# Performance work log

Hardware: AMD Instinct MI355X
Metric: run time of the kernel (lower is better)

Reference implementation:

```python
import jax, jax.numpy as jnp
import numpy as np
from jax import lax

T = 8
TAU = 2.0
ALPHA = 4.0   # spikingjelly surrogate.Sigmoid default alpha
EPS = 1e-5


def _kaiming(key, shape, fan_in):
    return jax.random.normal(key, shape, jnp.float32) * np.sqrt(2.0 / fan_in)


def setup_inputs() -> dict:
    key = jax.random.key(0)
    ks = jax.random.split(key, 16)
    d = {}
    d['x'] = jax.random.normal(ks[0], (128, 3, 32, 32), jnp.float32)
    convs = [('1', 32, 3), ('2', 32, 32), ('3', 64, 32), ('4', 64, 64), ('5', 128, 64), ('6', 128, 128)]
    for i, (s, co, ci) in enumerate(convs):
        d['w' + s] = _kaiming(ks[1 + i], (co, ci, 3, 3), ci * 9)
        d['b' + s] = jnp.zeros((co,), jnp.float32)
        d['g' + s] = jnp.ones((co,), jnp.float32)
        d['be' + s] = jnp.zeros((co,), jnp.float32)
    d['fc1_w'] = _kaiming(ks[7], (128, 2048), 2048)
    d['fc1_b'] = jnp.zeros((128,), jnp.float32)
    d['fc2_w'] = _kaiming(ks[8], (10, 128), 128)
    d['fc2_b'] = jnp.zeros((10,), jnp.float32)
    return d


def _conv2d(x, w, b):  # x [M,C,H,W], w [O,I,3,3], pad=1 stride=1
    y = lax.conv_general_dilated(x, w, (1, 1), ((1, 1), (1, 1)),
                                 dimension_numbers=('NCHW', 'OIHW', 'NCHW'))
    return y + b[None, :, None, None]


def _bn(x, g, be):  # training-mode BN over merged (T*N,H,W) batch
    m = x.mean(axis=(0, 2, 3))
    v = x.var(axis=(0, 2, 3))
    inv = g / jnp.sqrt(v + EPS)
    return x * inv[None, :, None, None] + (be - m * inv)[None, :, None, None]


def _lif(x_seq, th):
    # spikingjelly LIFNode defaults: decay_input=True, v_reset=0 (hard reset),
    # surrogate sigmoid gradient. x_seq: [T, ...]
    def step(v, x):
        v = v + (x - v) / TAU
        sig = jax.nn.sigmoid(ALPHA * (v - th))
        hard = (v >= th).astype(x.dtype)
        spike = lax.stop_gradient(hard - sig) + sig  # fwd: heaviside, bwd: sigmoid'
        return v * (1.0 - spike), spike
    return lax.scan(step, jnp.zeros_like(x_seq[0]), x_seq)[1]


def _maxpool(x):  # [M,C,H,W] -> 2x2 stride 2
    return lax.reduce_window(x, -jnp.inf, lax.max, (1, 1, 2, 2), (1, 1, 2, 2), 'VALID')


def _cbl(xs, w, b, g, be, th):  # conv-bn over merged TN, LIF scan over T
    t, n = xs.shape[0], xs.shape[1]
    m = xs.reshape((t * n,) + xs.shape[2:])
    y = _bn(_conv2d(m, w, b), g, be)
    return _lif(y.reshape((t, n) + y.shape[1:]), th)


def _pool_seq(xs):
    t, n = xs.shape[0], xs.shape[1]
    y = _maxpool(xs.reshape((t * n,) + xs.shape[2:]))
    return y.reshape((t, n) + y.shape[1:])


def _forward(x, w1, b1, g1, be1, w2, b2, g2, be2, w3, b3, g3, be3,
             w4, b4, g4, be4, w5, b5, g5, be5, w6, b6, g6, be6,
             fc1_w, fc1_b, fc2_w, fc2_b):
    th = 1.0
    xs = jnp.broadcast_to(x[None], (T,) + x.shape)  # [T,N,3,32,32]
    xs = _cbl(xs, w1, b1, g1, be1, th)
    xs = _cbl(xs, w2, b2, g2, be2, th)
    xs = _pool_seq(xs)                                # [T,N,32,16,16]
    xs = _cbl(xs, w3, b3, g3, be3, th)
    xs = _cbl(xs, w4, b4, g4, be4, th)
    xs = _pool_seq(xs)                                # [T,N,64,8,8]
    xs = _cbl(xs, w5, b5, g5, be5, th)
    xs = _cbl(xs, w6, b6, g6, be6, th)
    xs = _pool_seq(xs)                                # [T,N,128,4,4]
    t, n = xs.shape[0], xs.shape[1]
    f = xs.reshape(t, n, -1)                          # [T,N,2048]
    h = jnp.einsum('tnf,of->tno', f, fc1_w) + fc1_b
    h = _lif(h, 1.0)
    o = jnp.einsum('tnf,of->tno', h, fc2_w) + fc2_b
    o = _lif(o, 1.0)
    return o.mean(axis=0)                             # [N,10]


def reference(x, w1, b1, g1, be1, w2, b2, g2, be2, w3, b3, g3, be3,
              w4, b4, g4, be4, w5, b5, g5, be5, w6, b6, g6, be6,
              fc1_w, fc1_b, fc2_w, fc2_b):
    return _forward(x, w1, b1, g1, be1, w2, b2, g2, be2, w3, b3, g3, be3,
                    w4, b4, g4, be4, w5, b5, g5, be5, w6, b6, g6, be6,
                    fc1_w, fc1_b, fc2_w, fc2_b)
```

## Files before the change

kernel.cpp:

```cpp
#include <hip/hip_runtime.h>
#include <stdint.h>


#define T_STEPS 8
#define NBATCH 128

typedef __attribute__((ext_vector_type(8))) short short8;
typedef __attribute__((ext_vector_type(4))) float f32x4;

__device__ __forceinline__ uint16_t f2bf(float f) {
    uint32_t x = __float_as_uint(f);
    uint32_t r = x + 0x7FFFu + ((x >> 16) & 1u);
    return (uint16_t)(r >> 16);
}
__device__ __forceinline__ float bf2f(uint16_t h) {
    return __uint_as_float(((uint32_t)h) << 16);
}

__global__ void zero_kernel(float* p, int n) {
    int i = blockIdx.x * blockDim.x + threadIdx.x;
    if (i < n) p[i] = 0.0f;
}

template <int C, int HP, int WPP>
__global__ void border_kernel(uint16_t* __restrict__ s, int nimg) {
    constexpr int NB = 2 * WPP + 2 * (HP - 2);
    constexpr int C2 = C / 2;
    constexpr int PX = C + 8;
    const int i = blockIdx.x * blockDim.x + threadIdx.x;
    if (i >= nimg * NB * C2) return;
    const int c2 = i % C2;
    const int b = (i / C2) % NB;
    const int img = i / (C2 * NB);
    int py, px;
    if (b < WPP) { py = 0; px = b; }
    else if (b < 2 * WPP) { py = HP - 1; px = b - WPP; }
    else { const int r = b - 2 * WPP; py = 1 + (r >> 1); px = (r & 1) ? (WPP - 1) : 0; }
    *(uint32_t*)&s[(size_t)img * (HP * WPP * PX) + (py * WPP + px) * PX + 2 * c2] = 0u;
}

template <int CIN, int COUT>
__global__ void prep_kernel(const float* __restrict__ w, uint16_t* __restrict__ wp) {
    constexpr int KC = CIN / 32;
    const int i = blockIdx.x * blockDim.x + threadIdx.x;
    if (i >= COUT * CIN * 9) return;
    const int sh = i % 9;
    const int ci = (i / 9) % CIN;
    const int co = i / (9 * CIN);
    const float v = w[i];
    const uint16_t h1 = f2bf(v);
    const float r1 = v - bf2f(h1);
    const uint16_t h2 = f2bf(r1);
    const float r2 = r1 - bf2f(h2);
    const uint16_t h3 = f2bf(r2);
    uint16_t* base = wp + (size_t)((co >> 4) * KC + (ci >> 5)) * 14976
                        + sh * 1664 + (co & 15) * 104 + (ci & 31);
    base[0] = h1;
    base[32] = h2;
    base[64] = h3;
}

__global__ void prep_fc1_kernel(const float* __restrict__ w, uint16_t* __restrict__ wp) {
    const int i = blockIdx.x * blockDim.x + threadIdx.x;
    if (i >= 128 * 2048) return;
    const int kp = i & 2047;
    const int o = i >> 11;
    const int px = kp >> 7, c = kp & 127;
    const float v = w[o * 2048 + c * 16 + px];
    const uint16_t h1 = f2bf(v);
    const float r1 = v - bf2f(h1);
    const uint16_t h2 = f2bf(r1);
    const float r2 = r1 - bf2f(h2);
    const uint16_t h3 = f2bf(r2);
    uint16_t* base = wp + (size_t)((o >> 4) * 64 + (kp >> 5)) * 1664
                        + (o & 15) * 104 + (kp & 31);
    base[0] = h1;
    base[32] = h2;
    base[64] = h3;
}

__global__ void conv3x3_kernel(const float* __restrict__ in,
                               const float* __restrict__ wgt,
                               const float* __restrict__ bias,
                               float* __restrict__ y,
                               float* __restrict__ ssum,
                               float* __restrict__ ssq,
                               int Cin, int H, int W) {
    const int m  = blockIdx.x;
    const int co = blockIdx.y;
    const int Cout = gridDim.y;
    const int HW = H * W;

    const float* wco = wgt + (size_t)co * Cin * 9;
    const float bv = bias[co];

    float lsum = 0.0f, lsq = 0.0f;

    for (int p = threadIdx.x; p < HW; p += blockDim.x) {
        const int hy = p / W;
        const int wx = p - hy * W;
        float acc = bv;
        for (int ci = 0; ci < Cin; ++ci) {
            const float* inc = in + ((size_t)m * Cin + ci) * HW;
            const float* wc = wco + ci * 9;
#pragma unroll
            for (int ky = 0; ky < 3; ++ky) {
                const int iy = hy + ky - 1;
                if (iy < 0 || iy >= H) continue;
#pragma unroll
                for (int kx = 0; kx < 3; ++kx) {
                    const int ix = wx + kx - 1;
                    if (ix < 0 || ix >= W) continue;
                    acc += inc[iy * W + ix] * wc[ky * 3 + kx];
                }
            }
        }
        y[((size_t)m * HW + p) * Cout + co] = acc;
        lsum += acc;
        lsq += acc * acc;
    }

    __shared__ float r1[256];
    __shared__ float r2[256];
    const int tid = threadIdx.x;
    r1[tid] = lsum;
    r2[tid] = lsq;
    __syncthreads();
    for (int s = blockDim.x >> 1; s > 0; s >>= 1) {
        if (tid < s) {
            r1[tid] += r1[tid + s];
            r2[tid] += r2[tid + s];
        }
        __syncthreads();
    }
    if (tid == 0) {
        atomicAdd(&ssum[co], r1[0]);
        atomicAdd(&ssq[co], r2[0]);
    }
}

template <int CIN, int COUT, int H, int W, int ROWS, int IMPB, int NCO, int KSPLIT>
__global__ __launch_bounds__(256) void conv_mfma_kernel(
    const uint16_t* __restrict__ in, const uint16_t* __restrict__ wp,
    const float* __restrict__ bias, float* __restrict__ y,
    float* __restrict__ ssum, float* __restrict__ ssq)
{
    constexpr int KC = CIN / 32;
    constexpr int WPP = W + 2;
    constexpr int HW = H * W;
    constexpr int PXU16 = CIN + 8;
    constexpr int ISTR = (H + 2) * WPP * PXU16;
    constexpr int RB = H / ROWS;
    constexpr int NSTRIP = IMPB * ROWS * W / 16;
    constexpr int MSPLIT = 4 / KSPLIT;
    constexpr int SPW = NSTRIP / MSPLIT;
    constexpr int TILE_U16 = IMPB * (ROWS + 2) * WPP * PXU16;
    constexpr int NIT = KC * 9;
    constexpr int ITW = NIT / KSPLIT;
    constexpr int CS = NCO * 16 + 1;
    static_assert(IMPB == 1 || ROWS == H, "impb needs full-image tiles");
    static_assert(NSTRIP % MSPLIT == 0 && NSTRIP % 4 == 0, "strips");
    static_assert(NIT % KSPLIT == 0, "ksplit");
    static_assert(TILE_U16 % 8 == 0, "tile f4");
    static_assert(KSPLIT == 1 || TILE_U16 * 2 >= NSTRIP * 16 * CS * 4, "C fits");

    __shared__ __align__(16) uint16_t sp[TILE_U16];
    __shared__ float bn[NCO * 32];

    const int tid = threadIdx.x;
    const int lane = tid & 63;
    const int wav = tid >> 6;
    const int kg = wav / MSPLIT;
    const int mg = wav - kg * MSPLIT;
    const int col = lane & 15;
    const int quad = lane >> 4;

    const int m0 = (blockIdx.x / RB) * IMPB;
    const int ybase = (blockIdx.x % RB) * ROWS;

    if (tid < NCO * 32) bn[tid] = 0.0f;

    {
        const float4* src = (const float4*)(in + (size_t)m0 * ISTR
                                               + (size_t)ybase * WPP * PXU16);
        float4* dst = (float4*)sp;
        for (int i = tid; i < TILE_U16 / 8; i += 256) dst[i] = src[i];
    }
    __syncthreads();

    int abase[SPW];
#pragma unroll
    for (int s = 0; s < SPW; ++s) {
        const int p = (mg * SPW + s) * 16 + col;
        const int img = p / (ROWS * W);
        const int rem = p % (ROWS * W);
        abase[s] = ((img * (ROWS + 2) + rem / W) * WPP + rem % W) * PXU16 + quad * 8;
    }

    f32x4 acc[SPW][NCO];
#pragma unroll
    for (int s = 0; s < SPW; ++s)
#pragma unroll
        for (int j = 0; j < NCO; ++j) acc[s][j] = (f32x4)0.0f;

    const uint16_t* wbase = wp + ((size_t)blockIdx.y * NCO * KC) * 14976
                               + col * 104 + quad * 8;

    auto loadB = [&](short8 (&buf)[NCO][3], int it) {
        const int kc = it / 9, sh = it - kc * 9;
#pragma unroll
        for (int j = 0; j < NCO; ++j) {
            const uint16_t* p = wbase + (size_t)(j * KC + kc) * 14976 + sh * 1664;
            buf[j][0] = *(const short8*)p;
            buf[j][1] = *(const short8*)(p + 32);
            buf[j][2] = *(const short8*)(p + 64);
        }
    };
    auto mfmaStep = [&](short8 (&buf)[NCO][3], int it) {
        const int kc = it / 9, sh = it - kc * 9;
        const int dy = sh / 3, dx = sh - dy * 3;
        const int shoff = (dy * WPP + dx) * PXU16 + kc * 32;
#pragma unroll
        for (int s = 0; s < SPW; ++s) {
            const short8 a = *(const short8*)&sp[abase[s] + shoff];
#pragma unroll
            for (int j = 0; j < NCO; ++j) {
                f32x4 t = acc[s][j];
                t = __builtin_amdgcn_mfma_f32_16x16x32_bf16(a, buf[j][0], t, 0, 0, 0);
                t = __builtin_amdgcn_mfma_f32_16x16x32_bf16(a, buf[j][1], t, 0, 0, 0);
                t = __builtin_amdgcn_mfma_f32_16x16x32_bf16(a, buf[j][2], t, 0, 0, 0);
                acc[s][j] = t;
            }
        }
    };

    short8 bufA[NCO][3], bufB[NCO][3];
    const int it0 = kg * ITW, it1 = it0 + ITW;
    loadB(bufA, it0);
    int it = it0;
#pragma unroll 1
    for (; it + 2 <= it1; it += 2) {
        loadB(bufB, it + 1);
        mfmaStep(bufA, it);
        if (it + 2 < it1) loadB(bufA, it + 2);
        mfmaStep(bufB, it + 1);
    }
    if (it < it1) mfmaStep(bufA, it);

    if constexpr (KSPLIT == 1) {
#pragma unroll
        for (int j = 0; j < NCO; ++j) {
            const int co0 = (blockIdx.y * NCO + j) * 16;
            const float bv = bias[co0 + col];
#pragma unroll
            for (int s = 0; s < SPW; ++s) {
                const int pb_ = (mg * SPW + s) * 16 + quad * 4;
                float sum = 0.0f, sq = 0.0f;
#pragma unroll
                for (int r = 0; r < 4; ++r) {
                    const float v = acc[s][j][r] + bv;
                    const int p = pb_ + r;
                    const int img = p / (ROWS * W);
                    const int pxim = p % (ROWS * W) + ybase * W;
                    y[((size_t)(m0 + img) * HW + pxim) * COUT + co0 + col] = v;
                    sum += v;
                    sq += v * v;
                }
                sum += __shfl_xor(sum, 16, 64);
                sum += __shfl_xor(sum, 32, 64);
                sq += __shfl_xor(sq, 16, 64);
                sq += __shfl_xor(sq, 32, 64);
                if (quad == 0) {
                    atomicAdd(&bn[j * 32 + col], sum);
                    atomicAdd(&bn[j * 32 + 16 + col], sq);
                }
            }
        }
    } else {
        float* Csh = (float*)sp;
        __syncthreads();
        if (kg == 0) {
#pragma unroll
            for (int s = 0; s < SPW; ++s)
#pragma unroll
                for (int j = 0; j < NCO; ++j)
#pragma unroll
                    for (int r = 0; r < 4; ++r)
                        Csh[((mg * SPW + s) * 16 + quad * 4 + r) * CS + j * 16 + col]
                            = acc[s][j][r];
        }
        __syncthreads();
#pragma unroll
        for (int k = 1; k < KSPLIT; ++k) {
            if (kg == k) {
#pragma unroll
                for (int s = 0; s < SPW; ++s)
#pragma unroll
                    for (int j = 0; j < NCO; ++j)
#pragma unroll
                        for (int r = 0; r < 4; ++r)
                            Csh[((mg * SPW + s) * 16 + quad * 4 + r) * CS + j * 16 + col]
                                += acc[s][j][r];
            }
            __syncthreads();
        }
        constexpr int ES = NSTRIP / 4;
#pragma unroll
        for (int s2 = 0; s2 < ES; ++s2) {
            const int gs = wav * ES + s2;
#pragma unroll
            for (int j = 0; j < NCO; ++j) {
                const int co0 = (blockIdx.y * NCO + j) * 16;
                const float bv = bias[co0 + col];
                float sum = 0.0f, sq = 0.0f;
#pragma unroll
                for (int r = 0; r < 4; ++r) {
                    const float v = Csh[(gs * 16 + quad * 4 + r) * CS + j * 16 + col] + bv;
                    const int p = gs * 16 + quad * 4 + r;
                    const int img = p / (ROWS * W);
                    const int pxim = p % (ROWS * W) + ybase * W;
                    y[((size_t)(m0 + img) * HW + pxim) * COUT + co0 + col] = v;
                    sum += v;
                    sq += v * v;
                }
                sum += __shfl_xor(sum, 16, 64);
                sum += __shfl_xor(sum, 32, 64);
                sq += __shfl_xor(sq, 16, 64);
                sq += __shfl_xor(sq, 32, 64);
                if (quad == 0) {
                    atomicAdd(&bn[j * 32 + col], sum);
                    atomicAdd(&bn[j * 32 + 16 + col], sq);
                }
            }
        }
    }
    __syncthreads();
    if (tid < NCO * 32) {
        const int j = tid >> 5, r = tid & 31;
        const int co0 = (blockIdx.y * NCO + j) * 16;
        if (r < 16) atomicAdd(&ssum[co0 + r], bn[j * 32 + r]);
        else atomicAdd(&ssq[co0 + r - 16], bn[j * 32 + r]);
    }
}

__global__ void bnlif1_pad_kernel(const float* __restrict__ y,
                                  const float* __restrict__ ssum,
                                  const float* __restrict__ ssq,
                                  const float* __restrict__ g,
                                  const float* __restrict__ be,
                                  uint16_t* __restrict__ s, float invM) {
    constexpr int OSTR = 34 * 34 * 40;
    const int i = blockIdx.x * blockDim.x + threadIdx.x;
    if (i >= NBATCH * 1024 * 16) return;
    const int c2 = i % 16;
    const int px = (i / 16) % 1024;
    const int n = i / (16 * 1024);
    const int c0 = 2 * c2;
    const float m0 = ssum[c0] * invM, m1 = ssum[c0 + 1] * invM;
    const float inv0 = g[c0] / sqrtf(ssq[c0] * invM - m0 * m0 + 1e-5f);
    const float inv1 = g[c0 + 1] / sqrtf(ssq[c0 + 1] * invM - m1 * m1 + 1e-5f);
    const float2 zz = *(const float2*)&y[((size_t)n * 1024 + px) * 32 + c0];
    const float z0 = zz.x * inv0 + (be[c0] - m0 * inv0);
    const float z1 = zz.y * inv1 + (be[c0 + 1] - m1 * inv1);
    const int pyy = px >> 5, pxx = px & 31;
    const size_t obase = (size_t)n * OSTR + ((pyy + 1) * 34 + pxx + 1) * 40 + c0;
    const size_t otstride = (size_t)NBATCH * OSTR;
    float v0 = 0.0f, v1 = 0.0f;
#pragma unroll
    for (int t = 0; t < T_STEPS; ++t) {
        v0 += (z0 - v0) * 0.5f;
        v1 += (z1 - v1) * 0.5f;
        const uint32_t b0 = v0 >= 1.0f, b1 = v1 >= 1.0f;
        *(uint32_t*)&s[t * otstride + obase] = (b0 | (b1 << 16)) * 0x3F80u;
        if (b0) v0 = 0.0f;
        if (b1) v1 = 0.0f;
    }
}

template <int C, int H, int W>
__global__ void bnlif_pad_kernel(const float* __restrict__ y,
                                 const float* __restrict__ ssum,
                                 const float* __restrict__ ssq,
                                 const float* __restrict__ g,
                                 const float* __restrict__ be,
                                 uint16_t* __restrict__ s, float invM) {
    constexpr int C2 = C / 2;
    constexpr int HW = H * W;
    constexpr int OSTR = (H + 2) * (W + 2) * (C + 8);
    const int i = blockIdx.x * blockDim.x + threadIdx.x;
    if (i >= NBATCH * HW * C2) return;
    const int c2 = i % C2;
    const int px = (i / C2) % HW;
    const int n = i / (C2 * HW);
    const int c0 = 2 * c2;
    const float m0 = ssum[c0] * invM, m1 = ssum[c0 + 1] * invM;
    const float inv0 = g[c0] / sqrtf(ssq[c0] * invM - m0 * m0 + 1e-5f);
    const float inv1 = g[c0 + 1] / sqrtf(ssq[c0 + 1] * invM - m1 * m1 + 1e-5f);
    const float sh0 = be[c0] - m0 * inv0;
    const float sh1 = be[c0 + 1] - m1 * inv1;
    const size_t ybase = ((size_t)n * HW + px) * C + c0;
    const size_t tstride = (size_t)NBATCH * HW * C;
    const int pyy = px / W, pxx = px % W;
    const size_t obase = (size_t)n * OSTR + ((pyy + 1) * (W + 2) + pxx + 1) * (C + 8) + c0;
    const size_t otstride = (size_t)NBATCH * OSTR;
    float v0 = 0.0f, v1 = 0.0f;
#pragma unroll
    for (int t = 0; t < T_STEPS; ++t) {
        const float2 zz = *(const float2*)&y[t * tstride + ybase];
        const float z0 = zz.x * inv0 + sh0;
        const float z1 = zz.y * inv1 + sh1;
        v0 += (z0 - v0) * 0.5f;
        v1 += (z1 - v1) * 0.5f;
        const uint32_t b0 = v0 >= 1.0f, b1 = v1 >= 1.0f;
        *(uint32_t*)&s[t * otstride + obase] = (b0 | (b1 << 16)) * 0x3F80u;
        if (b0) v0 = 0.0f;
        if (b1) v1 = 0.0f;
    }
}

template <int C, int H, int W>
__global__ void bnlifpool_pad_kernel(const float* __restrict__ y,
                                     const float* __restrict__ ssum,
                                     const float* __restrict__ ssq,
                                     const float* __restrict__ g,
                                     const float* __restrict__ be,
                                     uint16_t* __restrict__ s, float invM) {
    constexpr int C2 = C / 2;
    constexpr int PH = H / 2, PW = W / 2;
    constexpr int OSTR = (PH + 2) * (PW + 2) * (C + 8);
    const int i = blockIdx.x * blockDim.x + threadIdx.x;
    if (i >= NBATCH * PH * PW * C2) return;
    const int c2 = i % C2;
    const int pw = (i / C2) % PW;
    const int ph = (i / (C2 * PW)) % PH;
    const int n = i / (C2 * PW * PH);
    const int c0 = 2 * c2;
    const float m0 = ssum[c0] * invM, m1 = ssum[c0 + 1] * invM;
    const float inv0 = g[c0] / sqrtf(ssq[c0] * invM - m0 * m0 + 1e-5f);
    const float inv1 = g[c0 + 1] / sqrtf(ssq[c0 + 1] * invM - m1 * m1 + 1e-5f);
    const float sh0 = be[c0] - m0 * inv0;
    const float sh1 = be[c0 + 1] - m1 * inv1;
    const size_t base = (((size_t)n * H + 2 * ph) * W + 2 * pw) * C + c0;
    const size_t tstride = (size_t)NBATCH * H * W * C;
    const size_t obase = (size_t)n * OSTR + ((ph + 1) * (PW + 2) + pw + 1) * (C + 8) + c0;
    const size_t otstride = (size_t)NBATCH * OSTR;
    float a0 = 0.f, a1 = 0.f, a2 = 0.f, a3 = 0.f;
    float b0_ = 0.f, b1_ = 0.f, b2_ = 0.f, b3_ = 0.f;
#pragma unroll
    for (int t = 0; t < T_STEPS; ++t) {
        const float* yt = y + t * tstride + base;
        const float2 p00 = *(const float2*)&yt[0];
        const float2 p01 = *(const float2*)&yt[C];
        const float2 p10 = *(const float2*)&yt[(size_t)W * C];
        const float2 p11 = *(const float2*)&yt[(size_t)W * C + C];
        a0 += (p00.x * inv0 + sh0 - a0) * 0.5f;
        a1 += (p01.x * inv0 + sh0 - a1) * 0.5f;
        a2 += (p10.x * inv0 + sh0 - a2) * 0.5f;
        a3 += (p11.x * inv0 + sh0 - a3) * 0.5f;
        b0_ += (p00.y * inv1 + sh1 - b0_) * 0.5f;
        b1_ += (p01.y * inv1 + sh1 - b1_) * 0.5f;
        b2_ += (p10.y * inv1 + sh1 - b2_) * 0.5f;
        b3_ += (p11.y * inv1 + sh1 - b3_) * 0.5f;
        const uint32_t sa0 = a0 >= 1.0f, sa1 = a1 >= 1.0f, sa2 = a2 >= 1.0f, sa3 = a3 >= 1.0f;
        const uint32_t sb0 = b0_ >= 1.0f, sb1 = b1_ >= 1.0f, sb2 = b2_ >= 1.0f, sb3 = b3_ >= 1.0f;
        if (sa0) a0 = 0.0f;
        if (sa1) a1 = 0.0f;
        if (sa2) a2 = 0.0f;
        if (sa3) a3 = 0.0f;
        if (sb0) b0_ = 0.0f;
        if (sb1) b1_ = 0.0f;
        if (sb2) b2_ = 0.0f;
        if (sb3) b3_ = 0.0f;
        const uint32_t pa = sa0 | sa1 | sa2 | sa3;
        const uint32_t pbt = sb0 | sb1 | sb2 | sb3;
        *(uint32_t*)&s[t * otstride + obase] = (pa | (pbt << 16)) * 0x3F80u;
    }
}

__global__ __launch_bounds__(256) void fc1_mfma_kernel(
    const uint16_t* __restrict__ f, const uint16_t* __restrict__ wfc,
    const float* __restrict__ b, float* __restrict__ h)
{
    __shared__ __align__(16) uint16_t A[16 * 2056];
    const int tid = threadIdx.x;
    const int lane = tid & 63, wav = tid >> 6;
    const int col = lane & 15, quad = lane >> 4;
    const int r0 = blockIdx.x * 16;

    {
        const int row = tid >> 4, px = tid & 15;
        const int py = px >> 2, pxx = px & 3;
        const float4* src = (const float4*)(f + (size_t)(r0 + row) * 4896
                                            + ((py + 1) * 6 + pxx + 1) * 136);
        float4* dst = (float4*)&A[row * 2056 + px * 128];
#pragma unroll
        for (int i = 0; i < 16; ++i) dst[i] = src[i];
    }
    __syncthreads();

    const int coblk = blockIdx.y * 4 + wav;
    const uint16_t* wbase = wfc + (size_t)coblk * 64 * 1664 + col * 104 + quad * 8;
    f32x4 acc = (f32x4)0.0f;

    auto loadB = [&](short8 (&buf)[3], int kc) {
        const uint16_t* p = wbase + kc * 1664;
        buf[0] = *(const short8*)p;
        buf[1] = *(const short8*)(p + 32);
        buf[2] = *(const short8*)(p + 64);
    };
    auto step = [&](short8 (&buf)[3], int kc) {
        const short8 a = *(const short8*)&A[col * 2056 + kc * 32 + quad * 8];
        acc = __builtin_amdgcn_mfma_f32_16x16x32_bf16(a, buf[0], acc, 0, 0, 0);
        acc = __builtin_amdgcn_mfma_f32_16x16x32_bf16(a, buf[1], acc, 0, 0, 0);
        acc = __builtin_amdgcn_mfma_f32_16x16x32_bf16(a, buf[2], acc, 0, 0, 0);
    };

    short8 bA[3], bB[3];
    loadB(bA, 0);
#pragma unroll 1
    for (int kc = 0; kc + 2 <= 64; kc += 2) {
        loadB(bB, kc + 1);
        step(bA, kc);
        if (kc + 2 < 64) loadB(bA, kc + 2);
        step(bB, kc + 1);
    }

    const int o = coblk * 16 + col;
    const float bv = b[o];
#pragma unroll
    for (int r = 0; r < 4; ++r)
        h[(size_t)(r0 + quad * 4 + r) * 128 + o] = acc[r] + bv;
}

__global__ void lif_fc_kernel(const float* __restrict__ h,
                              uint8_t* __restrict__ s, int NF) {
    const int i = blockIdx.x * blockDim.x + threadIdx.x;
    if (i >= NF) return;
    float v = 0.0f;
#pragma unroll
    for (int t = 0; t < T_STEPS; ++t) {
        const float z = h[(size_t)t * NF + i];
        v += (z - v) * 0.5f;
        const float sp = (v >= 1.0f) ? 1.0f : 0.0f;
        s[(size_t)t * NF + i] = (uint8_t)sp;
        v *= (1.0f - sp);
    }
}

__global__ void fc2_kernel(const uint8_t* __restrict__ sh,
                           const float* __restrict__ w,
                           const float* __restrict__ b,
                           float* __restrict__ out) {
    const int i = blockIdx.x * blockDim.x + threadIdx.x;
    if (i >= NBATCH * 10) return;
    const int k = i % 10;
    const int n = i / 10;
    float v = 0.0f, acc = 0.0f;
    for (int t = 0; t < T_STEPS; ++t) {
        const uint8_t* row = sh + ((size_t)t * NBATCH + n) * 128;
        float z = b[k];
        for (int o = 0; o < 128; ++o)
            z += (float)row[o] * w[k * 128 + o];
        v += (z - v) * 0.5f;
        const float sp = (v >= 1.0f) ? 1.0f : 0.0f;
        acc += sp;
        v *= (1.0f - sp);
    }
    out[i] = acc * (1.0f / T_STEPS);
}

extern "C" void kernel_launch(void* const* d_in, const int* in_sizes, int n_in,
                              void* d_out, int out_size, void* d_ws, size_t ws_size,
                              hipStream_t stream) {
    const float* x   = (const float*)d_in[0];
    const float* W1  = (const float*)d_in[1];
    const float* Bi1 = (const float*)d_in[2];
    const float* G1  = (const float*)d_in[3];
    const float* BE1 = (const float*)d_in[4];
    const float* W2  = (const float*)d_in[5];
    const float* Bi2 = (const float*)d_in[6];
    const float* G2  = (const float*)d_in[7];
    const float* BE2 = (const float*)d_in[8];
    const float* W3  = (const float*)d_in[9];
    const float* Bi3 = (const float*)d_in[10];
    const float* G3  = (const float*)d_in[11];
    const float* BE3 = (const float*)d_in[12];
    const float* W4  = (const float*)d_in[13];
    const float* Bi4 = (const float*)d_in[14];
    const float* G4  = (const float*)d_in[15];
    const float* BE4 = (const float*)d_in[16];
    const float* W5  = (const float*)d_in[17];
    const float* Bi5 = (const float*)d_in[18];
    const float* G5  = (const float*)d_in[19];
    const float* BE5 = (const float*)d_in[20];
    const float* W6  = (const float*)d_in[21];
    const float* Bi6 = (const float*)d_in[22];
    const float* G6  = (const float*)d_in[23];
    const float* BE6 = (const float*)d_in[24];
    const float* FC1W = (const float*)d_in[25];
    const float* FC1B = (const float*)d_in[26];
    const float* FC2W = (const float*)d_in[27];
    const float* FC2B = (const float*)d_in[28];

    uint8_t* ws = (uint8_t*)d_ws;
    float*    Y   = (float*)ws;
    const size_t S1OFF = 134217728;
    uint16_t* S1 = (uint16_t*)(ws + S1OFF);
    uint16_t* S2 = (uint16_t*)(ws + S1OFF);
    uint16_t* S3 = (uint16_t*)(ws + S1OFF + 26542080);
    uint16_t* S4 = (uint16_t*)(ws + S1OFF);
    uint16_t* S5 = (uint16_t*)(ws + S1OFF + 14745600);
    uint16_t* S6 = (uint16_t*)(ws + S1OFF + 42598400);
    float*    stats = (float*)(ws + S1OFF + 94699520);
    float*    h     = (float*)(ws + S1OFF + 94699520 + 8192);
    uint8_t*  shb   = ws + S1OFF + 94699520 + 8192 + 524288;
    uint16_t* Wp    = (uint16_t*)(shb + 131072);
    uint16_t* Wp2p = Wp;
    uint16_t* Wp3p = Wp + 29952;
    uint16_t* Wp4p = Wp + 89856;
    uint16_t* Wp5p = Wp + 209664;
    uint16_t* Wp6p = Wp + 449280;
    uint16_t* Wfc1 = Wp + 928512;

    zero_kernel<<<(1536 + 255) / 256, 256, 0, stream>>>(stats, 1536);

    prep_kernel<32, 32><<<(9216 + 255) / 256, 256, 0, stream>>>(W2, Wp2p);
    prep_kernel<32, 64><<<(18432 + 255) / 256, 256, 0, stream>>>(W3, Wp3p);
    prep_kernel<64, 64><<<(36864 + 255) / 256, 256, 0, stream>>>(W4, Wp4p);
    prep_kernel<64, 128><<<(73728 + 255) / 256, 256, 0, stream>>>(W5, Wp5p);
    prep_kernel<128, 128><<<(147456 + 255) / 256, 256, 0, stream>>>(W6, Wp6p);
    prep_fc1_kernel<<<(262144) / 256, 256, 0, stream>>>(FC1W, Wfc1);

    const int TN = T_STEPS * NBATCH;

    border_kernel<32, 34, 34><<<(1024 * 132 * 16 + 255) / 256, 256, 0, stream>>>(S1, 1024);
    border_kernel<32, 18, 18><<<(1024 * 68 * 16 + 255) / 256, 256, 0, stream>>>(S2, 1024);
    border_kernel<64, 18, 18><<<(1024 * 68 * 32 + 255) / 256, 256, 0, stream>>>(S3, 1024);
    border_kernel<64, 10, 10><<<(1024 * 36 * 32 + 255) / 256, 256, 0, stream>>>(S4, 1024);
    border_kernel<128, 10, 10><<<(1024 * 36 * 64 + 255) / 256, 256, 0, stream>>>(S5, 1024);
    border_kernel<128, 6, 6><<<(1024 * 20 * 64 + 255) / 256, 256, 0, stream>>>(S6, 1024);

    {
        dim3 g(NBATCH, 32);
        conv3x3_kernel<<<g, 256, 0, stream>>>(x, W1, Bi1, Y,
                                              stats + 0, stats + 128, 3, 32, 32);
        bnlif1_pad_kernel<<<(NBATCH * 1024 * 16 + 255) / 256, 256, 0, stream>>>(
            Y, stats + 0, stats + 128, G1, BE1, S1, 1.0f / 131072.0f);
    }
    {
        conv_mfma_kernel<32, 32, 32, 32, 16, 1, 2, 1><<<dim3(TN * 2, 1), 256, 0, stream>>>(
            S1, Wp2p, Bi2, Y, stats + 256, stats + 384);
        bnlifpool_pad_kernel<32, 32, 32><<<(NBATCH * 16 * 16 * 16 + 255) / 256, 256, 0, stream>>>(
            Y, stats + 256, stats + 384, G2, BE2, S2, 1.0f / (1024.0f * 1024.0f));
    }
    {
        conv_mfma_kernel<32, 64, 16, 16, 16, 2, 1, 1><<<dim3(TN / 2, 4), 256, 0, stream>>>(
            S2, Wp3p, Bi3, Y, stats + 512, stats + 640);
        bnlif_pad_kernel<64, 16, 16><<<(NBATCH * 256 * 32 + 255) / 256, 256, 0, stream>>>(
            Y, stats + 512, stats + 640, G3, BE3, S3, 1.0f / (1024.0f * 256.0f));
    }
    {
        conv_mfma_kernel<64, 64, 16, 16, 16, 1, 1, 2><<<dim3(TN, 4), 256, 0, stream>>>(
            S3, Wp4p, Bi4, Y, stats + 768, stats + 896);
        bnlifpool_pad_kernel<64, 16, 16><<<(NBATCH * 8 * 8 * 32 + 255) / 256, 256, 0, stream>>>(
            Y, stats + 768, stats + 896, G4, BE4, S4, 1.0f / (1024.0f * 256.0f));
    }
    {
        conv_mfma_kernel<64, 128, 8, 8, 8, 2, 2, 2><<<dim3(TN / 2, 4), 256, 0, stream>>>(
            S4, Wp5p, Bi5, Y, stats + 1024, stats + 1152);
        bnlif_pad_kernel<128, 8, 8><<<(NBATCH * 64 * 64 + 255) / 256, 256, 0, stream>>>(
            Y, stats + 1024, stats + 1152, G5, BE5, S5, 1.0f / (1024.0f * 64.0f));
    }
    {
        conv_mfma_kernel<128, 128, 8, 8, 8, 2, 2, 4><<<dim3(TN / 2, 4), 256, 0, stream>>>(
            S5, Wp6p, Bi6, Y, stats + 1280, stats + 1408);
        bnlifpool_pad_kernel<128, 8, 8><<<(NBATCH * 4 * 4 * 64 + 255) / 256, 256, 0, stream>>>(
            Y, stats + 1280, stats + 1408, G6, BE6, S6, 1.0f / (1024.0f * 64.0f));
    }
    fc1_mfma_kernel<<<dim3(64, 2), 256, 0, stream>>>(S6, Wfc1, FC1B, h);
    lif_fc_kernel<<<(NBATCH * 128 + 255) / 256, 256, 0, stream>>>(h, shb, NBATCH * 128);
    fc2_kernel<<<(NBATCH * 10 + 255) / 256, 256, 0, stream>>>(shb, FC2W, FC2B, (float*)d_out);
}
```

Before: 719.3 us.

## Store spike maps as packed bytes and expand to bf16 in shared memory

Spike activations between layers are now stored as one byte per channel with no channel padding, instead of bf16 with 8 extra channels per pixel. Conv and fc1 kernels read 16-byte chunks and expand each byte to bf16 0/1 while filling shared memory, and the BN/LIF kernels now handle four channels per thread. The weight-prep and border-zeroing launches are each merged into one kernel, and NCO is retuned for conv3/conv4. This cuts activation traffic to roughly half, at the cost of extra unpacking ALU work and shared-memory stores during tile loads.

New measurement: 691.7 us. 3.8% less time.

```diff
diff --git a/kernel.cpp b/kernel.cpp
--- a/kernel.cpp
+++ b/kernel.cpp
@@ -22,37 +22,22 @@
     if (i < n) p[i] = 0.0f;
 }
 
-template <int C, int HP, int WPP>
-__global__ void border_kernel(uint16_t* __restrict__ s, int nimg) {
-    constexpr int NB = 2 * WPP + 2 * (HP - 2);
-    constexpr int C2 = C / 2;
-    constexpr int PX = C + 8;
-    const int i = blockIdx.x * blockDim.x + threadIdx.x;
-    if (i >= nimg * NB * C2) return;
-    const int c2 = i % C2;
-    const int b = (i / C2) % NB;
-    const int img = i / (C2 * NB);
-    int py, px;
-    if (b < WPP) { py = 0; px = b; }
-    else if (b < 2 * WPP) { py = HP - 1; px = b - WPP; }
-    else { const int r = b - 2 * WPP; py = 1 + (r >> 1); px = (r & 1) ? (WPP - 1) : 0; }
-    *(uint32_t*)&s[(size_t)img * (HP * WPP * PX) + (py * WPP + px) * PX + 2 * c2] = 0u;
-}
-
-template <int CIN, int COUT>
-__global__ void prep_kernel(const float* __restrict__ w, uint16_t* __restrict__ wp) {
-    constexpr int KC = CIN / 32;
-    const int i = blockIdx.x * blockDim.x + threadIdx.x;
-    if (i >= COUT * CIN * 9) return;
+__device__ __forceinline__ void tsplit(float v, uint16_t& h1, uint16_t& h2, uint16_t& h3) {
+    h1 = f2bf(v);
+    const float r1 = v - bf2f(h1);
+    h2 = f2bf(r1);
+    const float r2 = r1 - bf2f(h2);
+    h3 = f2bf(r2);
+}
+
+__device__ __forceinline__ void prep_conv_one(const float* __restrict__ w,
+                                              uint16_t* __restrict__ wp, int i, int CIN) {
+    const int KC = CIN >> 5;
     const int sh = i % 9;
     const int ci = (i / 9) % CIN;
     const int co = i / (9 * CIN);
-    const float v = w[i];
-    const uint16_t h1 = f2bf(v);
-    const float r1 = v - bf2f(h1);
-    const uint16_t h2 = f2bf(r1);
-    const float r2 = r1 - bf2f(h2);
-    const uint16_t h3 = f2bf(r2);
+    uint16_t h1, h2, h3;
+    tsplit(w[i], h1, h2, h3);
     uint16_t* base = wp + (size_t)((co >> 4) * KC + (ci >> 5)) * 14976
                         + sh * 1664 + (co & 15) * 104 + (ci & 31);
     base[0] = h1;
@@ -60,23 +45,62 @@
     base[64] = h3;
 }
 
-__global__ void prep_fc1_kernel(const float* __restrict__ w, uint16_t* __restrict__ wp) {
-    const int i = blockIdx.x * blockDim.x + threadIdx.x;
-    if (i >= 128 * 2048) return;
+__device__ __forceinline__ void prep_fc1_one(const float* __restrict__ w,
+                                             uint16_t* __restrict__ wp, int i) {
     const int kp = i & 2047;
     const int o = i >> 11;
     const int px = kp >> 7, c = kp & 127;
-    const float v = w[o * 2048 + c * 16 + px];
-    const uint16_t h1 = f2bf(v);
-    const float r1 = v - bf2f(h1);
-    const uint16_t h2 = f2bf(r1);
-    const float r2 = r1 - bf2f(h2);
-    const uint16_t h3 = f2bf(r2);
+    uint16_t h1, h2, h3;
+    tsplit(w[o * 2048 + c * 16 + px], h1, h2, h3);
     uint16_t* base = wp + (size_t)((o >> 4) * 64 + (kp >> 5)) * 1664
                         + (o & 15) * 104 + (kp & 31);
     base[0] = h1;
     base[32] = h2;
     base[64] = h3;
+}
+
+__global__ void prep_all_kernel(const float* __restrict__ W2, const float* __restrict__ W3,
+                                const float* __restrict__ W4, const float* __restrict__ W5,
+                                const float* __restrict__ W6, const float* __restrict__ F1,
+                                uint16_t* __restrict__ P2, uint16_t* __restrict__ P3,
+                                uint16_t* __restrict__ P4, uint16_t* __restrict__ P5,
+                                uint16_t* __restrict__ P6, uint16_t* __restrict__ PF) {
+    int i = blockIdx.x * blockDim.x + threadIdx.x;
+    if (i < 9216) { prep_conv_one(W2, P2, i, 32); return; }
+    i -= 9216;
+    if (i < 18432) { prep_conv_one(W3, P3, i, 32); return; }
+    i -= 18432;
+    if (i < 36864) { prep_conv_one(W4, P4, i, 64); return; }
+    i -= 36864;
+    if (i < 73728) { prep_conv_one(W5, P5, i, 64); return; }
+    i -= 73728;
+    if (i < 147456) { prep_conv_one(W6, P6, i, 128); return; }
+    i -= 147456;
+    if (i < 262144) prep_fc1_one(F1, PF, i);
+}
+
+__global__ void border_all_kernel(uint8_t* S1, uint8_t* S2, uint8_t* S3,
+                                  uint8_t* S4, uint8_t* S5, uint8_t* S6) {
+    int i = blockIdx.x * blockDim.x + threadIdx.x;
+    uint8_t* s;
+    int C, HP, WPP;
+    if (i < 1081344) { s = S1; C = 32; HP = 34; WPP = 34; }
+    else if ((i -= 1081344) < 557056) { s = S2; C = 32; HP = 18; WPP = 18; }
+    else if ((i -= 557056) < 1114112) { s = S3; C = 64; HP = 18; WPP = 18; }
+    else if ((i -= 1114112) < 589824) { s = S4; C = 64; HP = 10; WPP = 10; }
+    else if ((i -= 589824) < 1179648) { s = S5; C = 128; HP = 10; WPP = 10; }
+    else if ((i -= 1179648) < 655360) { s = S6; C = 128; HP = 6; WPP = 6; }
+    else return;
+    const int C4 = C >> 2;
+    const int NB = 2 * WPP + 2 * (HP - 2);
+    const int c4 = i % C4;
+    const int b = (i / C4) % NB;
+    const int img = i / (C4 * NB);
+    int py, px;
+    if (b < WPP) { py = 0; px = b; }
+    else if (b < 2 * WPP) { py = HP - 1; px = b - WPP; }
+    else { const int r = b - 2 * WPP; py = 1 + (r >> 1); px = (r & 1) ? (WPP - 1) : 0; }
+    *(uint32_t*)&s[(size_t)img * (HP * WPP * C) + (py * WPP + px) * C + 4 * c4] = 0u;
 }
 
 __global__ void conv3x3_kernel(const float* __restrict__ in,
@@ -141,7 +165,7 @@
 
 template <int CIN, int COUT, int H, int W, int ROWS, int IMPB, int NCO, int KSPLIT>
 __global__ __launch_bounds__(256) void conv_mfma_kernel(
-    const uint16_t* __restrict__ in, const uint16_t* __restrict__ wp,
+    const uint8_t* __restrict__ in, const uint16_t* __restrict__ wp,
     const float* __restrict__ bias, float* __restrict__ y,
     float* __restrict__ ssum, float* __restrict__ ssq)
 {
@@ -149,19 +173,20 @@
     constexpr int WPP = W + 2;
     constexpr int HW = H * W;
     constexpr int PXU16 = CIN + 8;
-    constexpr int ISTR = (H + 2) * WPP * PXU16;
+    constexpr int ISTR_B = (H + 2) * WPP * CIN;
     constexpr int RB = H / ROWS;
     constexpr int NSTRIP = IMPB * ROWS * W / 16;
     constexpr int MSPLIT = 4 / KSPLIT;
     constexpr int SPW = NSTRIP / MSPLIT;
     constexpr int TILE_U16 = IMPB * (ROWS + 2) * WPP * PXU16;
+    constexpr int TILE_B = IMPB * (ROWS + 2) * WPP * CIN;
     constexpr int NIT = KC * 9;
     constexpr int ITW = NIT / KSPLIT;
     constexpr int CS = NCO * 16 + 1;
     static_assert(IMPB == 1 || ROWS == H, "impb needs full-image tiles");
     static_assert(NSTRIP % MSPLIT == 0 && NSTRIP % 4 == 0, "strips");
     static_assert(NIT % KSPLIT == 0, "ksplit");
-    static_assert(TILE_U16 % 8 == 0, "tile f4");
+    static_assert(TILE_B % 16 == 0, "tile u8 16B");
     static_assert(KSPLIT == 1 || TILE_U16 * 2 >= NSTRIP * 16 * CS * 4, "C fits");
 
     __shared__ __align__(16) uint16_t sp[TILE_U16];
@@ -181,10 +206,22 @@
     if (tid < NCO * 32) bn[tid] = 0.0f;
 
     {
-        const float4* src = (const float4*)(in + (size_t)m0 * ISTR
-                                               + (size_t)ybase * WPP * PXU16);
-        float4* dst = (float4*)sp;
-        for (int i = tid; i < TILE_U16 / 8; i += 256) dst[i] = src[i];
+        const uint8_t* src = in + (size_t)m0 * ISTR_B + (size_t)ybase * WPP * CIN;
+        for (int i = tid; i < TILE_B / 16; i += 256) {
+            const uint4 v = ((const uint4*)src)[i];
+            const int b = i * 16;
+            const int px = b / CIN;
+            const int ci = b - px * CIN;
+            uint32_t* d = (uint32_t*)&sp[px * PXU16 + ci];
+            d[0] = ((v.x & 1u) | (((v.x >> 8) & 1u) << 16)) * 0x3F80u;
+            d[1] = (((v.x >> 16) & 1u) | (((v.x >> 24) & 1u) << 16)) * 0x3F80u;
+            d[2] = ((v.y & 1u) | (((v.y >> 8) & 1u) << 16)) * 0x3F80u;
+            d[3] = (((v.y >> 16) & 1u) | (((v.y >> 24) & 1u) << 16)) * 0x3F80u;
+            d[4] = ((v.z & 1u) | (((v.z >> 8) & 1u) << 16)) * 0x3F80u;
+            d[5] = (((v.z >> 16) & 1u) | (((v.z >> 24) & 1u) << 16)) * 0x3F80u;
+            d[6] = ((v.w & 1u) | (((v.w >> 8) & 1u) << 16)) * 0x3F80u;
+            d[7] = (((v.w >> 16) & 1u) | (((v.w >> 24) & 1u) << 16)) * 0x3F80u;
+        }
     }
     __syncthreads();
 
@@ -348,32 +385,36 @@
                                   const float* __restrict__ ssq,
                                   const float* __restrict__ g,
                                   const float* __restrict__ be,
-                                  uint16_t* __restrict__ s, float invM) {
-    constexpr int OSTR = 34 * 34 * 40;
+                                  uint8_t* __restrict__ s, float invM) {
+    constexpr int OSTR = 34 * 34 * 32;
     const int i = blockIdx.x * blockDim.x + threadIdx.x;
-    if (i >= NBATCH * 1024 * 16) return;
-    const int c2 = i % 16;
-    const int px = (i / 16) % 1024;
-    const int n = i / (16 * 1024);
-    const int c0 = 2 * c2;
-    const float m0 = ssum[c0] * invM, m1 = ssum[c0 + 1] * invM;
-    const float inv0 = g[c0] / sqrtf(ssq[c0] * invM - m0 * m0 + 1e-5f);
-    const float inv1 = g[c0 + 1] / sqrtf(ssq[c0 + 1] * invM - m1 * m1 + 1e-5f);
-    const float2 zz = *(const float2*)&y[((size_t)n * 1024 + px) * 32 + c0];
-    const float z0 = zz.x * inv0 + (be[c0] - m0 * inv0);
-    const float z1 = zz.y * inv1 + (be[c0 + 1] - m1 * inv1);
+    if (i >= NBATCH * 1024 * 8) return;
+    const int c4 = i & 7;
+    const int px = (i >> 3) & 1023;
+    const int n = i >> 13;
+    const int c0 = 4 * c4;
+    float z[4], v[4];
+    const float4 q = *(const float4*)&y[((size_t)n * 1024 + px) * 32 + c0];
+    const float* qf = (const float*)&q;
+#pragma unroll
+    for (int c = 0; c < 4; ++c) {
+        const float m = ssum[c0 + c] * invM;
+        const float inv = g[c0 + c] / sqrtf(ssq[c0 + c] * invM - m * m + 1e-5f);
+        z[c] = qf[c] * inv + (be[c0 + c] - m * inv);
+        v[c] = 0.0f;
+    }
     const int pyy = px >> 5, pxx = px & 31;
-    const size_t obase = (size_t)n * OSTR + ((pyy + 1) * 34 + pxx + 1) * 40 + c0;
-    const size_t otstride = (size_t)NBATCH * OSTR;
-    float v0 = 0.0f, v1 = 0.0f;
+    const size_t obase = (size_t)n * OSTR + ((pyy + 1) * 34 + pxx + 1) * 32 + c0;
+    const size_t ot = (size_t)NBATCH * OSTR;
 #pragma unroll
     for (int t = 0; t < T_STEPS; ++t) {
-        v0 += (z0 - v0) * 0.5f;
-        v1 += (z1 - v1) * 0.5f;
-        const uint32_t b0 = v0 >= 1.0f, b1 = v1 >= 1.0f;
-        *(uint32_t*)&s[t * otstride + obase] = (b0 | (b1 << 16)) * 0x3F80u;
-        if (b0) v0 = 0.0f;
-        if (b1) v1 = 0.0f;
+        uint32_t pk = 0;
+#pragma unroll
+        for (int c = 0; c < 4; ++c) {
+            v[c] += (z[c] - v[c]) * 0.5f;
+            if (v[c] >= 1.0f) { v[c] = 0.0f; pk |= 1u << (8 * c); }
+        }
+        *(uint32_t*)&s[t * ot + obase] = pk;
     }
 }
 
@@ -383,38 +424,41 @@
                                  const float* __restrict__ ssq,
                                  const float* __restrict__ g,
                                  const float* __restrict__ be,
-                                 uint16_t* __restrict__ s, float invM) {
-    constexpr int C2 = C / 2;
+                                 uint8_t* __restrict__ s, float invM) {
+    constexpr int C4 = C / 4;
     constexpr int HW = H * W;
-    constexpr int OSTR = (H + 2) * (W + 2) * (C + 8);
+    constexpr int OSTR = (H + 2) * (W + 2) * C;
     const int i = blockIdx.x * blockDim.x + threadIdx.x;
-    if (i >= NBATCH * HW * C2) return;
-    const int c2 = i % C2;
-    const int px = (i / C2) % HW;
-    const int n = i / (C2 * HW);
-    const int c0 = 2 * c2;
-    const float m0 = ssum[c0] * invM, m1 = ssum[c0 + 1] * invM;
-    const float inv0 = g[c0] / sqrtf(ssq[c0] * invM - m0 * m0 + 1e-5f);
-    const float inv1 = g[c0 + 1] / sqrtf(ssq[c0 + 1] * invM - m1 * m1 + 1e-5f);
-    const float sh0 = be[c0] - m0 * inv0;
-    const float sh1 = be[c0 + 1] - m1 * inv1;
+    if (i >= NBATCH * HW * C4) return;
+    const int c4 = i % C4;
+    const int px = (i / C4) % HW;
+    const int n = i / (C4 * HW);
+    const int c0 = 4 * c4;
+    float inv[4], sh[4], v[4];
+#pragma unroll
+    for (int c = 0; c < 4; ++c) {
+        const float m = ssum[c0 + c] * invM;
+        inv[c] = g[c0 + c] / sqrtf(ssq[c0 + c] * invM - m * m + 1e-5f);
+        sh[c] = be[c0 + c] - m * inv[c];
+        v[c] = 0.0f;
+    }
     const size_t ybase = ((size_t)n * HW + px) * C + c0;
     const size_t tstride = (size_t)NBATCH * HW * C;
     const int pyy = px / W, pxx = px % W;
-    const size_t obase = (size_t)n * OSTR + ((pyy + 1) * (W + 2) + pxx + 1) * (C + 8) + c0;
-    const size_t otstride = (size_t)NBATCH * OSTR;
-    float v0 = 0.0f, v1 = 0.0f;
+    const size_t obase = (size_t)n * OSTR + ((pyy + 1) * (W + 2) + pxx + 1) * C + c0;
+    const size_t ot = (size_t)NBATCH * OSTR;
 #pragma unroll
     for (int t = 0; t < T_STEPS; ++t) {
-        const float2 zz = *(const float2*)&y[t * tstride + ybase];
-        const float z0 = zz.x * inv0 + sh0;
-        const float z1 = zz.y * inv1 + sh1;
-        v0 += (z0 - v0) * 0.5f;
-        v1 += (z1 - v1) * 0.5f;
-        const uint32_t b0 = v0 >= 1.0f, b1 = v1 >= 1.0f;
-        *(uint32_t*)&s[t * otstride + obase] = (b0 | (b1 << 16)) * 0x3F80u;
-        if (b0) v0 = 0.0f;
-        if (b1) v1 = 0.0f;
+        const float4 q = *(const float4*)&y[t * tstride + ybase];
+        const float* qf = (const float*)&q;
+        uint32_t pk = 0;
+#pragma unroll
+        for (int c = 0; c < 4; ++c) {
+            const float z = qf[c] * inv[c] + sh[c];
+            v[c] += (z - v[c]) * 0.5f;
+            if (v[c] >= 1.0f) { v[c] = 0.0f; pk |= 1u << (8 * c); }
+        }
+        *(uint32_t*)&s[t * ot + obase] = pk;
     }
 }
 
@@ -424,61 +468,55 @@
                                      const float* __restrict__ ssq,
                                      const float* __restrict__ g,
                                      const float* __restrict__ be,
-                                     uint16_t* __restrict__ s, float invM) {
-    constexpr int C2 = C / 2;
+                                     uint8_t* __restrict__ s, float invM) {
+    constexpr int C4 = C / 4;
     constexpr int PH = H / 2, PW = W / 2;
-    constexpr int OSTR = (PH + 2) * (PW + 2) * (C + 8);
+    constexpr int OSTR = (PH + 2) * (PW + 2) * C;
     const int i = blockIdx.x * blockDim.x + threadIdx.x;
-    if (i >= NBATCH * PH * PW * C2) return;
-    const int c2 = i % C2;
-    const int pw = (i / C2) % PW;
-    const int ph = (i / (C2 * PW)) % PH;
-    const int n = i / (C2 * PW * PH);
-    const int c0 = 2 * c2;
-    const float m0 = ssum[c0] * invM, m1 = ssum[c0 + 1] * invM;
-    const float inv0 = g[c0] / sqrtf(ssq[c0] * invM - m0 * m0 + 1e-5f);
-    const float inv1 = g[c0 + 1] / sqrtf(ssq[c0 + 1] * invM - m1 * m1 + 1e-5f);
-    const float sh0 = be[c0] - m0 * inv0;
-    const float sh1 = be[c0 + 1] - m1 * inv1;
+    if (i >= NBATCH * PH * PW * C4) return;
+    const int c4 = i % C4;
+    const int pw = (i / C4) % PW;
+    const int ph = (i / (C4 * PW)) % PH;
+    const int n = i / (C4 * PW * PH);
+    const int c0 = 4 * c4;
+    float inv[4], sh[4], v[4][4];
+#pragma unroll
+    for (int c = 0; c < 4; ++c) {
+        const float m = ssum[c0 + c] * invM;
+        inv[c] = g[c0 + c] / sqrtf(ssq[c0 + c] * invM - m * m + 1e-5f);
+        sh[c] = be[c0 + c] - m * inv[c];
+#pragma unroll
+        for (int p = 0; p < 4; ++p) v[p][c] = 0.0f;
+    }
     const size_t base = (((size_t)n * H + 2 * ph) * W + 2 * pw) * C + c0;
     const size_t tstride = (size_t)NBATCH * H * W * C;
-    const size_t obase = (size_t)n * OSTR + ((ph + 1) * (PW + 2) + pw + 1) * (C + 8) + c0;
-    const size_t otstride = (size_t)NBATCH * OSTR;
-    float a0 = 0.f, a1 = 0.f, a2 = 0.f, a3 = 0.f;
-    float b0_ = 0.f, b1_ = 0.f, b2_ = 0.f, b3_ = 0.f;
+    const size_t obase = (size_t)n * OSTR + ((ph + 1) * (PW + 2) + pw + 1) * C + c0;
+    const size_t ot = (size_t)NBATCH * OSTR;
 #pragma unroll
     for (int t = 0; t < T_STEPS; ++t) {
         const float* yt = y + t * tstride + base;
-        const float2 p00 = *(const float2*)&yt[0];
-        const float2 p01 = *(const float2*)&yt[C];
-        const float2 p10 = *(const float2*)&yt[(size_t)W * C];
-        const float2 p11 = *(const float2*)&yt[(size_t)W * C + C];
-        a0 += (p00.x * inv0 + sh0 - a0) * 0.5f;
-        a1 += (p01.x * inv0 + sh0 - a1) * 0.5f;
-        a2 += (p10.x * inv0 + sh0 - a2) * 0.5f;
-        a3 += (p11.x * inv0 + sh0 - a3) * 0.5f;
-        b0_ += (p00.y * inv1 + sh1 - b0_) * 0.5f;
-        b1_ += (p01.y * inv1 + sh1 - b1_) * 0.5f;
-        b2_ += (p10.y * inv1 + sh1 - b2_) * 0.5f;
-        b3_ += (p11.y * inv1 + sh1 - b3_) * 0.5f;
-        const uint32_t sa0 = a0 >= 1.0f, sa1 = a1 >= 1.0f, sa2 = a2 >= 1.0f, sa3 = a3 >= 1.0f;
-        const uint32_t sb0 = b0_ >= 1.0f, sb1 = b1_ >= 1.0f, sb2 = b2_ >= 1.0f, sb3 = b3_ >= 1.0f;
-        if (sa0) a0 = 0.0f;
-        if (sa1) a1 = 0.0f;
-        if (sa2) a2 = 0.0f;
-        if (sa3) a3 = 0.0f;
-        if (sb0) b0_ = 0.0f;
-        if (sb1) b1_ = 0.0f;
-        if (sb2) b2_ = 0.0f;
-        if (sb3) b3_ = 0.0f;
-        const uint32_t pa = sa0 | sa1 | sa2 | sa3;
-        const uint32_t pbt = sb0 | sb1 | sb2 | sb3;
-        *(uint32_t*)&s[t * otstride + obase] = (pa | (pbt << 16)) * 0x3F80u;
+        float4 q[4];
+        q[0] = *(const float4*)&yt[0];
+        q[1] = *(const float4*)&yt[C];
+        q[2] = *(const float4*)&yt[(size_t)W * C];
+        q[3] = *(const float4*)&yt[(size_t)W * C + C];
+        uint32_t pk = 0;
+#pragma unroll
+        for (int p = 0; p < 4; ++p) {
+            const float* qf = (const float*)&q[p];
+#pragma unroll
+            for (int c = 0; c < 4; ++c) {
+                const float z = qf[c] * inv[c] + sh[c];
+                v[p][c] += (z - v[p][c]) * 0.5f;
+                if (v[p][c] >= 1.0f) { v[p][c] = 0.0f; pk |= 1u << (8 * c); }
+            }
+        }
+        *(uint32_t*)&s[t * ot + obase] = pk;
     }
 }
 
 __global__ __launch_bounds__(256) void fc1_mfma_kernel(
-    const uint16_t* __restrict__ f, const uint16_t* __restrict__ wfc,
+    const uint8_t* __restrict__ f, const uint16_t* __restrict__ wfc,
     const float* __restrict__ b, float* __restrict__ h)
 {
     __shared__ __align__(16) uint16_t A[16 * 2056];
@@ -490,11 +528,21 @@
     {
         const int row = tid >> 4, px = tid & 15;
         const int py = px >> 2, pxx = px & 3;
-        const float4* src = (const float4*)(f + (size_t)(r0 + row) * 4896
-                                            + ((py + 1) * 6 + pxx + 1) * 136);
-        float4* dst = (float4*)&A[row * 2056 + px * 128];
-#pragma unroll
-        for (int i = 0; i < 16; ++i) dst[i] = src[i];
+        const uint8_t* src = f + (size_t)(r0 + row) * 4608
+                             + ((py + 1) * 6 + pxx + 1) * 128;
+        uint32_t* dst = (uint32_t*)&A[row * 2056 + px * 128];
+#pragma unroll
+        for (int i = 0; i < 8; ++i) {
+            const uint4 v = ((const uint4*)src)[i];
+            dst[8 * i + 0] = ((v.x & 1u) | (((v.x >> 8) & 1u) << 16)) * 0x3F80u;
+            dst[8 * i + 1] = (((v.x >> 16) & 1u) | (((v.x >> 24) & 1u) << 16)) * 0x3F80u;
+            dst[8 * i + 2] = ((v.y & 1u) | (((v.y >> 8) & 1u) << 16)) * 0x3F80u;
+            dst[8 * i + 3] = (((v.y >> 16) & 1u) | (((v.y >> 24) & 1u) << 16)) * 0x3F80u;
+            dst[8 * i + 4] = ((v.z & 1u) | (((v.z >> 8) & 1u) << 16)) * 0x3F80u;
+            dst[8 * i + 5] = (((v.z >> 16) & 1u) | (((v.z >> 24) & 1u) << 16)) * 0x3F80u;
+            dst[8 * i + 6] = ((v.w & 1u) | (((v.w >> 8) & 1u) << 16)) * 0x3F80u;
+            dst[8 * i + 7] = (((v.w >> 16) & 1u) | (((v.w >> 24) & 1u) << 16)) * 0x3F80u;
+        }
     }
     __syncthreads();
 
@@ -603,18 +651,18 @@
     const float* FC2B = (const float*)d_in[28];
 
     uint8_t* ws = (uint8_t*)d_ws;
-    float*    Y   = (float*)ws;
-    const size_t S1OFF = 134217728;
-    uint16_t* S1 = (uint16_t*)(ws + S1OFF);
-    uint16_t* S2 = (uint16_t*)(ws + S1OFF);
-    uint16_t* S3 = (uint16_t*)(ws + S1OFF + 26542080);
-    uint16_t* S4 = (uint16_t*)(ws + S1OFF);
-    uint16_t* S5 = (uint16_t*)(ws + S1OFF + 14745600);
-    uint16_t* S6 = (uint16_t*)(ws + S1OFF + 42598400);
-    float*    stats = (float*)(ws + S1OFF + 94699520);
-    float*    h     = (float*)(ws + S1OFF + 94699520 + 8192);
-    uint8_t*  shb   = ws + S1OFF + 94699520 + 8192 + 524288;
-    uint16_t* Wp    = (uint16_t*)(shb + 131072);
+    float*   Y  = (float*)ws;
+    const size_t SOFF = 134217728;
+    uint8_t* S1 = ws + SOFF;
+    uint8_t* S2 = ws + SOFF;
+    uint8_t* S3 = ws + SOFF + 10616832;
+    uint8_t* S4 = ws + SOFF;
+    uint8_t* S5 = ws + SOFF + 6553600;
+    uint8_t* S6 = ws + SOFF + 19660800;
+    float*   stats = (float*)(ws + SOFF + 37879808);
+    float*   h     = (float*)(ws + SOFF + 37879808 + 8192);
+    uint8_t* shb   = ws + SOFF + 37879808 + 8192 + 524288;
+    uint16_t* Wp   = (uint16_t*)(shb + 131072);
     uint16_t* Wp2p = Wp;
     uint16_t* Wp3p = Wp + 29952;
     uint16_t* Wp4p = Wp + 89856;
@@ -623,58 +671,47 @@
     uint16_t* Wfc1 = Wp + 928512;
 
     zero_kernel<<<(1536 + 255) / 256, 256, 0, stream>>>(stats, 1536);
-
-    prep_kernel<32, 32><<<(9216 + 255) / 256, 256, 0, stream>>>(W2, Wp2p);
-    prep_kernel<32, 64><<<(18432 + 255) / 256, 256, 0, stream>>>(W3, Wp3p);
-    prep_kernel<64, 64><<<(36864 + 255) / 256, 256, 0, stream>>>(W4, Wp4p);
-    prep_kernel<64, 128><<<(73728 + 255) / 256, 256, 0, stream>>>(W5, Wp5p);
-    prep_kernel<128, 128><<<(147456 + 255) / 256, 256, 0, stream>>>(W6, Wp6p);
-    prep_fc1_kernel<<<(262144) / 256, 256, 0, stream>>>(FC1W, Wfc1);
+    prep_all_kernel<<<(547840 + 255) / 256, 256, 0, stream>>>(
+        W2, W3, W4, W5, W6, FC1W, Wp2p, Wp3p, Wp4p, Wp5p, Wp6p, Wfc1);
+    border_all_kernel<<<(5177344 + 255) / 256, 256, 0, stream>>>(S1, S2, S3, S4, S5, S6);
 
     const int TN = T_STEPS * NBATCH;
-
-    border_kernel<32, 34, 34><<<(1024 * 132 * 16 + 255) / 256, 256, 0, stream>>>(S1, 1024);
-    border_kernel<32, 18, 18><<<(1024 * 68 * 16 + 255) / 256, 256, 0, stream>>>(S2, 1024);
-    border_kernel<64, 18, 18><<<(1024 * 68 * 32 + 255) / 256, 256, 0, stream>>>(S3, 1024);
-    border_kernel<64, 10, 10><<<(1024 * 36 * 32 + 255) / 256, 256, 0, stream>>>(S4, 1024);
-    border_kernel<128, 10, 10><<<(1024 * 36 * 64 + 255) / 256, 256, 0, stream>>>(S5, 1024);
-    border_kernel<128, 6, 6><<<(1024 * 20 * 64 + 255) / 256, 256, 0, stream>>>(S6, 1024);
 
     {
         dim3 g(NBATCH, 32);
         conv3x3_kernel<<<g, 256, 0, stream>>>(x, W1, Bi1, Y,
                                               stats + 0, stats + 128, 3, 32, 32);
-        bnlif1_pad_kernel<<<(NBATCH * 1024 * 16 + 255) / 256, 256, 0, stream>>>(
+        bnlif1_pad_kernel<<<(NBATCH * 1024 * 8) / 256, 256, 0, stream>>>(
             Y, stats + 0, stats + 128, G1, BE1, S1, 1.0f / 131072.0f);
     }
     {
         conv_mfma_kernel<32, 32, 32, 32, 16, 1, 2, 1><<<dim3(TN * 2, 1), 256, 0, stream>>>(
             S1, Wp2p, Bi2, Y, stats + 256, stats + 384);
-        bnlifpool_pad_kernel<32, 32, 32><<<(NBATCH * 16 * 16 * 16 + 255) / 256, 256, 0, stream>>>(
+        bnlifpool_pad_kernel<32, 32, 32><<<(NBATCH * 16 * 16 * 8) / 256, 256, 0, stream>>>(
             Y, stats + 256, stats + 384, G2, BE2, S2, 1.0f / (1024.0f * 1024.0f));
     }
     {
-        conv_mfma_kernel<32, 64, 16, 16, 16, 2, 1, 1><<<dim3(TN / 2, 4), 256, 0, stream>>>(
+        conv_mfma_kernel<32, 64, 16, 16, 16, 2, 2, 1><<<dim3(TN / 2, 2), 256, 0, stream>>>(
             S2, Wp3p, Bi3, Y, stats + 512, stats + 640);
-        bnlif_pad_kernel<64, 16, 16><<<(NBATCH * 256 * 32 + 255) / 256, 256, 0, stream>>>(
+        bnlif_pad_kernel<64, 16, 16><<<(NBATCH * 256 * 16) / 256, 256, 0, stream>>>(
             Y, stats + 512, stats + 640, G3, BE3, S3, 1.0f / (1024.0f * 256.0f));
     }
     {
-        conv_mfma_kernel<64, 64, 16, 16, 16, 1, 1, 2><<<dim3(TN, 4), 256, 0, stream>>>(
+        conv_mfma_kernel<64, 64, 16, 16, 16, 1, 2, 2><<<dim3(TN, 2), 256, 0, stream>>>(
             S3, Wp4p, Bi4, Y, stats + 768, stats + 896);
-        bnlifpool_pad_kernel<64, 16, 16><<<(NBATCH * 8 * 8 * 32 + 255) / 256, 256, 0, stream>>>(
+        bnlifpool_pad_kernel<64, 16, 16><<<(NBATCH * 8 * 8 * 16) / 256, 256, 0, stream>>>(
             Y, stats + 768, stats + 896, G4, BE4, S4, 1.0f / (1024.0f * 256.0f));
     }
     {
         conv_mfma_kernel<64, 128, 8, 8, 8, 2, 2, 2><<<dim3(TN / 2, 4), 256, 0, stream>>>(
             S4, Wp5p, Bi5, Y, stats + 1024, stats + 1152);
-        bnlif_pad_kernel<128, 8, 8><<<(NBATCH * 64 * 64 + 255) / 256, 256, 0, stream>>>(
+        bnlif_pad_kernel<128, 8, 8><<<(NBATCH * 64 * 32) / 256, 256, 0, stream>>>(
             Y, stats + 1024, stats + 1152, G5, BE5, S5, 1.0f / (1024.0f * 64.0f));
     }
     {
         conv_mfma_kernel<128, 128, 8, 8, 8, 2, 2, 4><<<dim3(TN / 2, 4), 256, 0, stream>>>(
             S5, Wp6p, Bi6, Y, stats + 1280, stats + 1408);
-        bnlifpool_pad_kernel<128, 8, 8><<<(NBATCH * 4 * 4 * 64 + 255) / 256, 256, 0, stream>>>(
+        bnlifpool_pad_kernel<128, 8, 8><<<(NBATCH * 4 * 4 * 32) / 256, 256, 0, stream>>>(
             Y, stats + 1280, stats + 1408, G6, BE6, S6, 1.0f / (1024.0f * 64.0f));
     }
     fc1_mfma_kernel<<<dim3(64, 2), 256, 0, stream>>>(S6, Wfc1, FC1B, h);
```
